# Performance work log

Hardware: AMD Instinct MI355X
Metric: run time of the kernel (lower is better)

Reference implementation:

```python
import jax, jax.numpy as jnp
import numpy as np

N = 100000   # nodes
E = 500000   # edges
D = 128      # h_dim
R = 230      # relation types ('num_edges' in __init__)
B = 64       # num_bases
SI = D // B  # submat_in = 2
SO = D // B  # submat_out = 2
L = 2        # n_hidden_layers
RRELU_SLOPE = (1.0 / 8.0 + 1.0 / 3.0) / 2.0  # F.rrelu eval-mode negative slope


def setup_inputs() -> dict:
    key = jax.random.key(0)
    ks = jax.random.split(key, 9)
    ent_embeds = jax.random.normal(ks[0], (N, D), jnp.float32)
    rel_embeds = jax.random.normal(ks[1], (R, D), jnp.float32)
    # xavier_normal-ish scale for per-relation basis weights and self-loop weights
    weight = jax.random.normal(ks[2], (L, R, B * SI * SO), jnp.float32) * 0.1
    loop_weight = jax.random.normal(ks[3], (L, D, D), jnp.float32) * (2.0 / np.sqrt(2 * D))
    norm = jax.random.uniform(ks[4], (N, 1), jnp.float32)
    node_id = jax.random.randint(ks[5], (N,), 0, N)
    edge_type = jax.random.randint(ks[6], (E,), 0, R)
    src = jax.random.randint(ks[7], (E,), 0, N)
    dst = jax.random.randint(ks[8], (E,), 0, N)
    return dict(ent_embeds=ent_embeds, rel_embeds=rel_embeds, weight=weight,
                loop_weight=loop_weight, norm=norm, node_id=node_id,
                edge_type=edge_type, src=src, dst=dst)


def reference(ent_embeds, rel_embeds, weight, loop_weight, norm,
              node_id, edge_type, src, dst):
    # Aggregator.forward: h = ent_embeds[g.ndata['id']]
    h = ent_embeds[node_id]  # [N, D]
    # (rel_embeds are gathered into g.edata['h'] but unused by RGCNLayer)
    for l in range(L):
        # msg_func: per-edge basis-block weight gather + block-diag bmm
        w = weight[l][edge_type].reshape(E, B, SI, SO)   # [E, B, 2, 2]
        node = h[src].reshape(E, B, SI)                  # [E, B, 2]
        msg = jnp.einsum('ebi,ebio->ebo', node, w).reshape(E, D)
        # update_all scatter-sum + apply_func norm multiply
        agg = jax.ops.segment_sum(msg, dst, num_segments=N) * norm
        # self-loop message (dropout=0)
        agg = agg + h @ loop_weight[l]
        # F.rrelu in eval mode: leaky with slope (lower+upper)/2
        h = jnp.where(agg >= 0, agg, agg * RRELU_SLOPE)
    return h
```

## Files before the change

kernel.cpp:

```cpp
#include <hip/hip_runtime.h>
#include <hip/hip_bf16.h>

#define NN 100000
#define NE 500000
#define DD 128
#define RR 230
#define SLOPE 0.2291666666666666667f

typedef __attribute__((ext_vector_type(8))) short short8;
typedef __attribute__((ext_vector_type(4))) float f32x4;

__device__ __forceinline__ short f2bf(float f) {
    unsigned u = __float_as_uint(f);
    u += 0x7fffu + ((u >> 16) & 1u);
    return (short)(u >> 16);
}
__device__ __forceinline__ unsigned pkbf(float lo, float hi) {
    return (unsigned)(unsigned short)f2bf(lo) | ((unsigned)(unsigned short)f2bf(hi) << 16);
}

#if defined(__has_builtin)
#if __has_builtin(__builtin_amdgcn_fdot2_f32_bf16)
#define HAS_DOT2 1
#endif
#endif
__device__ __forceinline__ void dot2acc(float& acc, unsigned x, unsigned w) {
#ifdef HAS_DOT2
    typedef __attribute__((ext_vector_type(2))) __bf16 bf16x2;
    acc = __builtin_amdgcn_fdot2_f32_bf16(__builtin_bit_cast(bf16x2, x),
                                          __builtin_bit_cast(bf16x2, w), acc, false);
#else
    acc = fmaf(__uint_as_float(x << 16),        __uint_as_float(w << 16),
          fmaf(__uint_as_float(x & 0xFFFF0000u), __uint_as_float(w & 0xFFFF0000u), acc));
#endif
}

__global__ __launch_bounds__(256) void hprep_k(const float* __restrict__ ent,
                                               const int* __restrict__ nid,
                                               unsigned short* __restrict__ hb) {
    int gid = blockIdx.x * 256 + threadIdx.x;
    if (gid >= (NN + 1) * 16) return;
    int n = gid >> 4;
    int u = gid & 15;
    short8 v = {0, 0, 0, 0, 0, 0, 0, 0};
    if (n < NN) {
        const float* srcp = ent + (size_t)nid[n] * DD + u * 8;
        float4 f0 = *(const float4*)srcp;
        float4 f1 = *(const float4*)(srcp + 4);
        v[0] = f2bf(f0.x); v[1] = f2bf(f0.y); v[2] = f2bf(f0.z); v[3] = f2bf(f0.w);
        v[4] = f2bf(f1.x); v[5] = f2bf(f1.y); v[6] = f2bf(f1.z); v[7] = f2bf(f1.w);
    }
    *(short8*)(hb + (size_t)n * DD + u * 8) = v;
}

__global__ __launch_bounds__(256) void hist_k(const int* __restrict__ dst,
                                              int* __restrict__ cnt) {
    int e = blockIdx.x * 256 + threadIdx.x;
    if (e >= NE) return;
    atomicAdd(&cnt[dst[e]], 1);
}

__global__ __launch_bounds__(256) void scan1_k(const int* __restrict__ cnt,
                                               int* __restrict__ off,
                                               int* __restrict__ bsum) {
    __shared__ int sh[256];
    int i = blockIdx.x * 256 + threadIdx.x;
    int v = (i < NN) ? cnt[i] : 0;
    sh[threadIdx.x] = v;
    __syncthreads();
    for (int d = 1; d < 256; d <<= 1) {
        int t = (threadIdx.x >= d) ? sh[threadIdx.x - d] : 0;
        __syncthreads();
        sh[threadIdx.x] += t;
        __syncthreads();
    }
    if (i < NN) off[i] = sh[threadIdx.x] - v;
    if (threadIdx.x == 255) bsum[blockIdx.x] = sh[255];
}

__global__ __launch_bounds__(512) void scan2_k(int* __restrict__ bsum, int nb) {
    __shared__ int sh[512];
    int v = (threadIdx.x < nb) ? bsum[threadIdx.x] : 0;
    sh[threadIdx.x] = v;
    __syncthreads();
    for (int d = 1; d < 512; d <<= 1) {
        int t = (threadIdx.x >= d) ? sh[threadIdx.x - d] : 0;
        __syncthreads();
        sh[threadIdx.x] += t;
        __syncthreads();
    }
    if (threadIdx.x < nb) bsum[threadIdx.x] = sh[threadIdx.x] - v;
}

__global__ __launch_bounds__(256) void scan3_k(int* __restrict__ off,
                                               const int* __restrict__ bsum,
                                               int* __restrict__ cursor) {
    int i = blockIdx.x * 256 + threadIdx.x;
    if (i < NN) {
        int o = off[i] + bsum[blockIdx.x];
        off[i] = o;
        cursor[i] = o;
    }
    if (i == 0) off[NN] = NE;
}

__global__ __launch_bounds__(256) void scat_k(const int* __restrict__ src,
                                              const int* __restrict__ et,
                                              const int* __restrict__ dst,
                                              int* __restrict__ cursor,
                                              int* __restrict__ epack) {
    int e = blockIdx.x * 256 + threadIdx.x;
    if (e >= NE) return;
    int pos = atomicAdd(&cursor[dst[e]], 1);
    epack[pos] = (src[e] << 8) | et[e];
}

__global__ __launch_bounds__(256) void wbprep_k(const float* __restrict__ weight,
                                                unsigned* __restrict__ wb) {
    int gid = blockIdx.x * 256 + threadIdx.x;
    if (gid >= 2 * RR * 32) return;
    int lt = gid >> 5;
    int hl = gid & 31;
    const float* wsrc = weight + (size_t)lt * 256 + hl * 8;
    float4 f0 = *(const float4*)wsrc;
    float4 f1 = *(const float4*)(wsrc + 4);
    uint4 v;
    v.x = pkbf(f0.x, f0.z);
    v.y = pkbf(f0.y, f0.w);
    v.z = pkbf(f1.x, f1.z);
    v.w = pkbf(f1.y, f1.w);
    *(uint4*)(wb + (size_t)lt * 128 + hl * 4) = v;
}

__global__ __launch_bounds__(256) void wprep_k(const float* __restrict__ lw,
                                               short* __restrict__ wt) {
    int gid = blockIdx.x * 256 + threadIdx.x;
    if (gid >= 2 * DD * 16) return;
    int l   = gid >> 11;
    int rem = gid & 2047;
    int c   = rem >> 4;
    int u   = rem & 15;
    const float* wsrc = lw + l * DD * DD + c;
    short8 v;
    #pragma unroll
    for (int j = 0; j < 8; ++j) v[j] = f2bf(wsrc[(u * 8 + j) * DD]);
    *(short8*)(wt + (size_t)l * DD * DD + c * DD + ((u ^ (c & 7)) << 3)) = v;
}

#define ZP (NN << 8)
__global__ __launch_bounds__(256) void agg_k(const unsigned short* __restrict__ hb,
                                             const int* __restrict__ off,
                                             const int* __restrict__ epack,
                                             const unsigned* __restrict__ wb,
                                             const float* __restrict__ norm,
                                             unsigned short* __restrict__ aggb) {
    int n    = (blockIdx.x * 256 + threadIdx.x) >> 6;
    int lane = threadIdx.x & 63;
    int hl   = lane & 31;
    int h2   = lane >> 5;
    if (n >= NN) return;
    int e0 = off[n];
    int m  = off[n + 1] - e0;
    float a0 = 0.f, a1 = 0.f, a2 = 0.f, a3 = 0.f;
    const char* hbb = (const char*)hb;
    const char* wbb = (const char*)wb;
    const int hoff = hl * 8;
    const int woff = hl * 16;

    for (int base = 0; base < m; base += 64) {
        int cnt = m - base;
        if (cnt > 64) cnt = 64;
        int pv = epack[e0 + base + ((lane < cnt) ? lane : 0)];

        for (int j = 0; j < cnt; j += 8) {
            int i0 = j + h2, i1 = j + 2 + h2, i2 = j + 4 + h2, i3 = j + 6 + h2;
            int p0 = (i0 < cnt) ? __shfl(pv, i0) : ZP;
            int p1 = (i1 < cnt) ? __shfl(pv, i1) : ZP;
            int p2 = (i2 < cnt) ? __shfl(pv, i2) : ZP;
            int p3 = (i3 < cnt) ? __shfl(pv, i3) : ZP;
            uint2 x0 = *(const uint2*)(hbb + (p0 & 0xFFFFFF00u) + hoff);
            uint2 x1 = *(const uint2*)(hbb + (p1 & 0xFFFFFF00u) + hoff);
            uint2 x2 = *(const uint2*)(hbb + (p2 & 0xFFFFFF00u) + hoff);
            uint2 x3 = *(const uint2*)(hbb + (p3 & 0xFFFFFF00u) + hoff);
            uint4 w0 = *(const uint4*)(wbb + ((p0 & 255) << 9) + woff);
            uint4 w1 = *(const uint4*)(wbb + ((p1 & 255) << 9) + woff);
            uint4 w2 = *(const uint4*)(wbb + ((p2 & 255) << 9) + woff);
            uint4 w3 = *(const uint4*)(wbb + ((p3 & 255) << 9) + woff);
            dot2acc(a0, x0.x, w0.x); dot2acc(a1, x0.x, w0.y);
            dot2acc(a2, x0.y, w0.z); dot2acc(a3, x0.y, w0.w);
            dot2acc(a0, x1.x, w1.x); dot2acc(a1, x1.x, w1.y);
            dot2acc(a2, x1.y, w1.z); dot2acc(a3, x1.y, w1.w);
            dot2acc(a0, x2.x, w2.x); dot2acc(a1, x2.x, w2.y);
            dot2acc(a2, x2.y, w2.z); dot2acc(a3, x2.y, w2.w);
            dot2acc(a0, x3.x, w3.x); dot2acc(a1, x3.x, w3.y);
            dot2acc(a2, x3.y, w3.z); dot2acc(a3, x3.y, w3.w);
        }
    }
    a0 += __shfl_xor(a0, 32);
    a1 += __shfl_xor(a1, 32);
    a2 += __shfl_xor(a2, 32);
    a3 += __shfl_xor(a3, 32);
    if (h2 == 0) {
        float nv = norm[n];
        uint2 pk;
        pk.x = pkbf(a0 * nv, a1 * nv);
        pk.y = pkbf(a2 * nv, a3 * nv);
        *(uint2*)(aggb + (size_t)n * DD + hl * 4) = pk;
    }
}

template<int WRITE_BF16>
__global__ __launch_bounds__(256, 2) void apply_k(const unsigned short* __restrict__ aggb,
                                                  const unsigned short* __restrict__ hb,
                                                  const short* __restrict__ Wt,
                                                  float* __restrict__ outf,
                                                  unsigned short* __restrict__ outb) {
    __shared__ short Ash[DD * DD];
    __shared__ short Wsh[DD * DD];

    const int tid = threadIdx.x;
    const long n0 = (long)blockIdx.x * 128;

    {
        const float4* wsrc = (const float4*)Wt;
        float4*       wdst = (float4*)Wsh;
        #pragma unroll
        for (int i = 0; i < 8; ++i) wdst[tid + i * 256] = wsrc[tid + i * 256];
    }
    {
        const int r  = tid >> 1;
        const int hf = tid & 1;
        long srow = n0 + r;
        if (srow >= NN) srow = NN - 1;
        const unsigned short* hrow = hb + (size_t)srow * DD + hf * 64;
        short* arow = Ash + r * DD;
        #pragma unroll
        for (int uu = 0; uu < 8; ++uu) {
            int u = hf * 8 + uu;
            short8 v = *(const short8*)(hrow + uu * 8);
            *(short8*)(arow + ((u ^ (r & 7)) << 3)) = v;
        }
    }
    __syncthreads();

    const int wv  = tid >> 6;
    const int wm  = wv >> 1;
    const int wn  = wv & 1;
    const int l16 = tid & 15;
    const int q   = (tid & 63) >> 4;

    f32x4 acc[4][4];
    #pragma unroll
    for (int mt = 0; mt < 4; ++mt)
        #pragma unroll
        for (int nt = 0; nt < 4; ++nt) acc[mt][nt] = (f32x4){0.f, 0.f, 0.f, 0.f};

    union Frag { uint2 u2[2]; short8 s8; };

    #pragma unroll
    for (int ks = 0; ks < 4; ++ks) {
        const int ua   = ks * 4 + (q >> 1);
        const int off8 = 4 * (q & 1);
        short8 af[4], bf[4];
        #pragma unroll
        for (int mt = 0; mt < 4; ++mt) {
            int r = wm * 64 + mt * 16 + l16;
            const short* base = Ash + r * DD;
            Frag fr;
            fr.u2[0] = *(const uint2*)(base + ((ua       ^ (r & 7)) << 3) + off8);
            fr.u2[1] = *(const uint2*)(base + (((ua + 2) ^ (r & 7)) << 3) + off8);
            af[mt] = fr.s8;
        }
        #pragma unroll
        for (int nt = 0; nt < 4; ++nt) {
            int c = wn * 64 + nt * 16 + l16;
            const short* base = Wsh + c * DD;
            Frag fr;
            fr.u2[0] = *(const uint2*)(base + ((ua       ^ (c & 7)) << 3) + off8);
            fr.u2[1] = *(const uint2*)(base + (((ua + 2) ^ (c & 7)) << 3) + off8);
            bf[nt] = fr.s8;
        }
        #pragma unroll
        for (int mt = 0; mt < 4; ++mt)
            #pragma unroll
            for (int nt = 0; nt < 4; ++nt)
                acc[mt][nt] = __builtin_amdgcn_mfma_f32_16x16x32_bf16(
                                  af[mt], bf[nt], acc[mt][nt], 0, 0, 0);
    }

    #pragma unroll
    for (int mt = 0; mt < 4; ++mt) {
        #pragma unroll
        for (int i = 0; i < 4; ++i) {
            long nrow = n0 + wm * 64 + mt * 16 + 4 * q + i;
            if (nrow < NN) {
                #pragma unroll
                for (int nt = 0; nt < 4; ++nt) {
                    int c = wn * 64 + nt * 16 + l16;
                    float g = __uint_as_float((unsigned)aggb[nrow * DD + c] << 16);
                    float v = g + acc[mt][nt][i];
                    v = (v >= 0.f) ? v : v * SLOPE;
                    if (WRITE_BF16) outb[nrow * DD + c] = (unsigned short)f2bf(v);
                    else            outf[nrow * DD + c] = v;
                }
            }
        }
    }
}

extern "C" void kernel_launch(void* const* d_in, const int* in_sizes, int n_in,
                              void* d_out, int out_size, void* d_ws, size_t ws_size,
                              hipStream_t stream) {
    const float* ent_embeds  = (const float*)d_in[0];
    const float* weight      = (const float*)d_in[2];
    const float* loop_weight = (const float*)d_in[3];
    const float* norm        = (const float*)d_in[4];
    const int*   node_id     = (const int*)d_in[5];
    const int*   edge_type   = (const int*)d_in[6];
    const int*   src         = (const int*)d_in[7];
    const int*   dst         = (const int*)d_in[8];
    float*       out         = (float*)d_out;

    unsigned short* aggb = (unsigned short*)d_ws;
    unsigned short* hb   = aggb + (size_t)NN * DD;
    int*   cnt    = (int*)(hb + (size_t)(NN + 1) * DD);
    int*   off    = cnt + NN;
    int*   cursor = off + NN + 1;
    int*   bsum   = cursor + NN;
    int*   epack  = bsum + 512;
    short* wt     = (short*)(epack + NE);
    unsigned* wb  = (unsigned*)(wt + 2 * DD * DD);

    const int NB_E = (NE + 255) / 256;
    const int NB_N = (NN + 255) / 256;

    hipMemsetAsync(cnt, 0, (size_t)NN * sizeof(int), stream);
    wprep_k <<<16, 256, 0, stream>>>(loop_weight, wt);
    wbprep_k<<<(2 * RR * 32 + 255) / 256, 256, 0, stream>>>(weight, wb);
    hprep_k <<<((NN + 1) * 16 + 255) / 256, 256, 0, stream>>>(ent_embeds, node_id, hb);
    hist_k  <<<NB_E, 256, 0, stream>>>(dst, cnt);
    scan1_k <<<NB_N, 256, 0, stream>>>(cnt, off, bsum);
    scan2_k <<<1,    512, 0, stream>>>(bsum, NB_N);
    scan3_k <<<NB_N, 256, 0, stream>>>(off, bsum, cursor);
    scat_k  <<<NB_E, 256, 0, stream>>>(src, edge_type, dst, cursor, epack);

    const int AGG_BLOCKS = (NN * 64) / 256;
    const int APL_BLOCKS = (NN + 127) / 128;

    agg_k     <<<AGG_BLOCKS, 256, 0, stream>>>(hb, off, epack, wb, norm, aggb);
    apply_k<1><<<APL_BLOCKS, 256, 0, stream>>>(aggb, hb, wt, nullptr, hb);

    agg_k     <<<AGG_BLOCKS, 256, 0, stream>>>(hb, off, epack, wb + (size_t)RR * 128,
                                               norm, aggb);
    apply_k<0><<<APL_BLOCKS, 256, 0, stream>>>(aggb, hb, wt + (size_t)DD * DD, out, nullptr);
}
```

Before: 212.5 us.

## Merge prep kernels, fuse scan stages, pad CSR segments to multiples of eight

Four preprocessing kernels (loop-weight transpose, basis-weight pack, h gather/convert, degree histogram) are merged into one launch that also fills a padded edge buffer with a zero-row sentinel. The scan now rounds each node's degree up to a multiple of eight, and the second and third scan stages are folded into one kernel where each block reduces the preceding block sums itself. The aggregation loop drops its per-64 chunking and bounds checks, loading eight packed edges per step and relying on the sentinel padding. The aim is fewer launches and a simpler inner loop, at the cost of a larger edge buffer, an extra fill pass and wasted work on padded slots.

```diff
diff --git a/kernel.cpp b/kernel.cpp
--- a/kernel.cpp
+++ b/kernel.cpp
@@ -6,6 +6,9 @@
 #define DD 128
 #define RR 230
 #define SLOPE 0.2291666666666666667f
+
+#define EPMAX (NE + 7 * NN)
+#define ZP (NN << 8)
 
 typedef __attribute__((ext_vector_type(8))) short short8;
 typedef __attribute__((ext_vector_type(4))) float f32x4;
@@ -35,29 +38,73 @@
 #endif
 }
 
-__global__ __launch_bounds__(256) void hprep_k(const float* __restrict__ ent,
-                                               const int* __restrict__ nid,
-                                               unsigned short* __restrict__ hb) {
-    int gid = blockIdx.x * 256 + threadIdx.x;
-    if (gid >= (NN + 1) * 16) return;
-    int n = gid >> 4;
-    int u = gid & 15;
-    short8 v = {0, 0, 0, 0, 0, 0, 0, 0};
-    if (n < NN) {
-        const float* srcp = ent + (size_t)nid[n] * DD + u * 8;
-        float4 f0 = *(const float4*)srcp;
-        float4 f1 = *(const float4*)(srcp + 4);
-        v[0] = f2bf(f0.x); v[1] = f2bf(f0.y); v[2] = f2bf(f0.z); v[3] = f2bf(f0.w);
-        v[4] = f2bf(f1.x); v[5] = f2bf(f1.y); v[6] = f2bf(f1.z); v[7] = f2bf(f1.w);
-    }
-    *(short8*)(hb + (size_t)n * DD + u * 8) = v;
-}
-
-__global__ __launch_bounds__(256) void hist_k(const int* __restrict__ dst,
-                                              int* __restrict__ cnt) {
-    int e = blockIdx.x * 256 + threadIdx.x;
-    if (e >= NE) return;
-    atomicAdd(&cnt[dst[e]], 1);
+#define P1_WT_E   16
+#define P1_WB_E   74
+#define P1_FL_E   (74 + (EPMAX / 4 + 255) / 256)
+#define P1_HB_E   (P1_FL_E + ((NN + 1) * 16 + 255) / 256)
+#define P1_TOT    (P1_HB_E + (NE + 255) / 256)
+
+__global__ __launch_bounds__(256) void p1_k(const float* __restrict__ lw,
+                                            const float* __restrict__ weight,
+                                            const float* __restrict__ ent,
+                                            const int* __restrict__ nid,
+                                            const int* __restrict__ dst,
+                                            short* __restrict__ wt,
+                                            unsigned* __restrict__ wb,
+                                            unsigned short* __restrict__ hb,
+                                            int* __restrict__ epack,
+                                            int* __restrict__ cnt) {
+    int bid = blockIdx.x;
+    if (bid < P1_WT_E) {
+        int gid = bid * 256 + threadIdx.x;
+        if (gid >= 2 * DD * 16) return;
+        int l   = gid >> 11;
+        int rem = gid & 2047;
+        int c   = rem >> 4;
+        int u   = rem & 15;
+        const float* wsrc = lw + l * DD * DD + c;
+        short8 v;
+        #pragma unroll
+        for (int j = 0; j < 8; ++j) v[j] = f2bf(wsrc[(u * 8 + j) * DD]);
+        *(short8*)(wt + (size_t)l * DD * DD + c * DD + ((u ^ (c & 7)) << 3)) = v;
+    } else if (bid < P1_WB_E) {
+        int gid = (bid - P1_WT_E) * 256 + threadIdx.x;
+        if (gid >= 2 * RR * 32) return;
+        int lt = gid >> 5;
+        int hl = gid & 31;
+        const float* wsrc = weight + (size_t)lt * 256 + hl * 8;
+        float4 f0 = *(const float4*)wsrc;
+        float4 f1 = *(const float4*)(wsrc + 4);
+        uint4 v;
+        v.x = pkbf(f0.x, f0.z);
+        v.y = pkbf(f0.y, f0.w);
+        v.z = pkbf(f1.x, f1.z);
+        v.w = pkbf(f1.y, f1.w);
+        *(uint4*)(wb + (size_t)lt * 128 + hl * 4) = v;
+    } else if (bid < P1_FL_E) {
+        int idx = (bid - P1_WB_E) * 256 + threadIdx.x;
+        if (idx * 4 >= EPMAX) return;
+        int4 z = make_int4(ZP, ZP, ZP, ZP);
+        *(int4*)(epack + idx * 4) = z;
+    } else if (bid < P1_HB_E) {
+        int gid = (bid - P1_FL_E) * 256 + threadIdx.x;
+        if (gid >= (NN + 1) * 16) return;
+        int n = gid >> 4;
+        int u = gid & 15;
+        short8 v = {0, 0, 0, 0, 0, 0, 0, 0};
+        if (n < NN) {
+            const float* srcp = ent + (size_t)nid[n] * DD + u * 8;
+            float4 f0 = *(const float4*)srcp;
+            float4 f1 = *(const float4*)(srcp + 4);
+            v[0] = f2bf(f0.x); v[1] = f2bf(f0.y); v[2] = f2bf(f0.z); v[3] = f2bf(f0.w);
+            v[4] = f2bf(f1.x); v[5] = f2bf(f1.y); v[6] = f2bf(f1.z); v[7] = f2bf(f1.w);
+        }
+        *(short8*)(hb + (size_t)n * DD + u * 8) = v;
+    } else {
+        int e = (bid - P1_HB_E) * 256 + threadIdx.x;
+        if (e >= NE) return;
+        atomicAdd(&cnt[dst[e]], 1);
+    }
 }
 
 __global__ __launch_bounds__(256) void scan1_k(const int* __restrict__ cnt,
@@ -65,7 +112,7 @@
                                                int* __restrict__ bsum) {
     __shared__ int sh[256];
     int i = blockIdx.x * 256 + threadIdx.x;
-    int v = (i < NN) ? cnt[i] : 0;
+    int v = (i < NN) ? ((cnt[i] + 7) & ~7) : 0;
     sh[threadIdx.x] = v;
     __syncthreads();
     for (int d = 1; d < 256; d <<= 1) {
@@ -78,30 +125,31 @@
     if (threadIdx.x == 255) bsum[blockIdx.x] = sh[255];
 }
 
-__global__ __launch_bounds__(512) void scan2_k(int* __restrict__ bsum, int nb) {
-    __shared__ int sh[512];
-    int v = (threadIdx.x < nb) ? bsum[threadIdx.x] : 0;
-    sh[threadIdx.x] = v;
+__global__ __launch_bounds__(256) void scan23_k(int* __restrict__ off,
+                                                const int* __restrict__ bsum,
+                                                int* __restrict__ cursor,
+                                                int nb) {
+    __shared__ int sh[256];
+    const int bid = blockIdx.x;
+    const int tid = threadIdx.x;
+    int s = 0;
+    if (tid < bid) s = bsum[tid];
+    if (tid + 256 < bid) s += bsum[tid + 256];
+    sh[tid] = s;
     __syncthreads();
-    for (int d = 1; d < 512; d <<= 1) {
-        int t = (threadIdx.x >= d) ? sh[threadIdx.x - d] : 0;
+    #pragma unroll
+    for (int d = 128; d > 0; d >>= 1) {
+        if (tid < d) sh[tid] += sh[tid + d];
         __syncthreads();
-        sh[threadIdx.x] += t;
-        __syncthreads();
-    }
-    if (threadIdx.x < nb) bsum[threadIdx.x] = sh[threadIdx.x] - v;
-}
-
-__global__ __launch_bounds__(256) void scan3_k(int* __restrict__ off,
-                                               const int* __restrict__ bsum,
-                                               int* __restrict__ cursor) {
-    int i = blockIdx.x * 256 + threadIdx.x;
+    }
+    const int S = sh[0];
+    int i = bid * 256 + tid;
     if (i < NN) {
-        int o = off[i] + bsum[blockIdx.x];
+        int o = off[i] + S;
         off[i] = o;
         cursor[i] = o;
     }
-    if (i == 0) off[NN] = NE;
+    if (bid == nb - 1 && tid == 0) off[NN] = S + bsum[bid];
 }
 
 __global__ __launch_bounds__(256) void scat_k(const int* __restrict__ src,
@@ -115,39 +163,6 @@
     epack[pos] = (src[e] << 8) | et[e];
 }
 
-__global__ __launch_bounds__(256) void wbprep_k(const float* __restrict__ weight,
-                                                unsigned* __restrict__ wb) {
-    int gid = blockIdx.x * 256 + threadIdx.x;
-    if (gid >= 2 * RR * 32) return;
-    int lt = gid >> 5;
-    int hl = gid & 31;
-    const float* wsrc = weight + (size_t)lt * 256 + hl * 8;
-    float4 f0 = *(const float4*)wsrc;
-    float4 f1 = *(const float4*)(wsrc + 4);
-    uint4 v;
-    v.x = pkbf(f0.x, f0.z);
-    v.y = pkbf(f0.y, f0.w);
-    v.z = pkbf(f1.x, f1.z);
-    v.w = pkbf(f1.y, f1.w);
-    *(uint4*)(wb + (size_t)lt * 128 + hl * 4) = v;
-}
-
-__global__ __launch_bounds__(256) void wprep_k(const float* __restrict__ lw,
-                                               short* __restrict__ wt) {
-    int gid = blockIdx.x * 256 + threadIdx.x;
-    if (gid >= 2 * DD * 16) return;
-    int l   = gid >> 11;
-    int rem = gid & 2047;
-    int c   = rem >> 4;
-    int u   = rem & 15;
-    const float* wsrc = lw + l * DD * DD + c;
-    short8 v;
-    #pragma unroll
-    for (int j = 0; j < 8; ++j) v[j] = f2bf(wsrc[(u * 8 + j) * DD]);
-    *(short8*)(wt + (size_t)l * DD * DD + c * DD + ((u ^ (c & 7)) << 3)) = v;
-}
-
-#define ZP (NN << 8)
 __global__ __launch_bounds__(256) void agg_k(const unsigned short* __restrict__ hb,
                                              const int* __restrict__ off,
                                              const int* __restrict__ epack,
@@ -161,47 +176,39 @@
     if (n >= NN) return;
     int e0 = off[n];
     int m  = off[n + 1] - e0;
+    float nv = norm[n];
     float a0 = 0.f, a1 = 0.f, a2 = 0.f, a3 = 0.f;
-    const char* hbb = (const char*)hb;
-    const char* wbb = (const char*)wb;
-    const int hoff = hl * 8;
-    const int woff = hl * 16;
-
-    for (int base = 0; base < m; base += 64) {
-        int cnt = m - base;
-        if (cnt > 64) cnt = 64;
-        int pv = epack[e0 + base + ((lane < cnt) ? lane : 0)];
-
-        for (int j = 0; j < cnt; j += 8) {
-            int i0 = j + h2, i1 = j + 2 + h2, i2 = j + 4 + h2, i3 = j + 6 + h2;
-            int p0 = (i0 < cnt) ? __shfl(pv, i0) : ZP;
-            int p1 = (i1 < cnt) ? __shfl(pv, i1) : ZP;
-            int p2 = (i2 < cnt) ? __shfl(pv, i2) : ZP;
-            int p3 = (i3 < cnt) ? __shfl(pv, i3) : ZP;
-            uint2 x0 = *(const uint2*)(hbb + (p0 & 0xFFFFFF00u) + hoff);
-            uint2 x1 = *(const uint2*)(hbb + (p1 & 0xFFFFFF00u) + hoff);
-            uint2 x2 = *(const uint2*)(hbb + (p2 & 0xFFFFFF00u) + hoff);
-            uint2 x3 = *(const uint2*)(hbb + (p3 & 0xFFFFFF00u) + hoff);
-            uint4 w0 = *(const uint4*)(wbb + ((p0 & 255) << 9) + woff);
-            uint4 w1 = *(const uint4*)(wbb + ((p1 & 255) << 9) + woff);
-            uint4 w2 = *(const uint4*)(wbb + ((p2 & 255) << 9) + woff);
-            uint4 w3 = *(const uint4*)(wbb + ((p3 & 255) << 9) + woff);
-            dot2acc(a0, x0.x, w0.x); dot2acc(a1, x0.x, w0.y);
-            dot2acc(a2, x0.y, w0.z); dot2acc(a3, x0.y, w0.w);
-            dot2acc(a0, x1.x, w1.x); dot2acc(a1, x1.x, w1.y);
-            dot2acc(a2, x1.y, w1.z); dot2acc(a3, x1.y, w1.w);
-            dot2acc(a0, x2.x, w2.x); dot2acc(a1, x2.x, w2.y);
-            dot2acc(a2, x2.y, w2.z); dot2acc(a3, x2.y, w2.w);
-            dot2acc(a0, x3.x, w3.x); dot2acc(a1, x3.x, w3.y);
-            dot2acc(a2, x3.y, w3.z); dot2acc(a3, x3.y, w3.w);
-        }
+    const char* hbb = (const char*)hb + hl * 8;
+    const char* wbb = (const char*)wb + hl * 16;
+
+    for (int j = 0; j < m; j += 8) {
+        int pv = epack[e0 + j + (lane & 7)];
+        int p0 = __shfl(pv, h2);
+        int p1 = __shfl(pv, 2 + h2);
+        int p2 = __shfl(pv, 4 + h2);
+        int p3 = __shfl(pv, 6 + h2);
+        uint2 x0 = *(const uint2*)(hbb + (p0 & 0xFFFFFF00u));
+        uint2 x1 = *(const uint2*)(hbb + (p1 & 0xFFFFFF00u));
+        uint2 x2 = *(const uint2*)(hbb + (p2 & 0xFFFFFF00u));
+        uint2 x3 = *(const uint2*)(hbb + (p3 & 0xFFFFFF00u));
+        uint4 w0 = *(const uint4*)(wbb + ((p0 & 255) << 9));
+        uint4 w1 = *(const uint4*)(wbb + ((p1 & 255) << 9));
+        uint4 w2 = *(const uint4*)(wbb + ((p2 & 255) << 9));
+        uint4 w3 = *(const uint4*)(wbb + ((p3 & 255) << 9));
+        dot2acc(a0, x0.x, w0.x); dot2acc(a1, x0.x, w0.y);
+        dot2acc(a2, x0.y, w0.z); dot2acc(a3, x0.y, w0.w);
+        dot2acc(a0, x1.x, w1.x); dot2acc(a1, x1.x, w1.y);
+        dot2acc(a2, x1.y, w1.z); dot2acc(a3, x1.y, w1.w);
+        dot2acc(a0, x2.x, w2.x); dot2acc(a1, x2.x, w2.y);
+        dot2acc(a2, x2.y, w2.z); dot2acc(a3, x2.y, w2.w);
+        dot2acc(a0, x3.x, w3.x); dot2acc(a1, x3.x, w3.y);
+        dot2acc(a2, x3.y, w3.z); dot2acc(a3, x3.y, w3.w);
     }
     a0 += __shfl_xor(a0, 32);
     a1 += __shfl_xor(a1, 32);
     a2 += __shfl_xor(a2, 32);
     a3 += __shfl_xor(a3, 32);
     if (h2 == 0) {
-        float nv = norm[n];
         uint2 pk;
         pk.x = pkbf(a0 * nv, a1 * nv);
         pk.y = pkbf(a2 * nv, a3 * nv);
@@ -326,22 +333,19 @@
     int*   cnt    = (int*)(hb + (size_t)(NN + 1) * DD);
     int*   off    = cnt + NN;
     int*   cursor = off + NN + 1;
-    int*   bsum   = cursor + NN;
-    int*   epack  = bsum + 512;
-    short* wt     = (short*)(epack + NE);
+    int*   epack  = cursor + NN;
+    int*   bsum   = epack + EPMAX;
+    short* wt     = (short*)(bsum + 512);
     unsigned* wb  = (unsigned*)(wt + 2 * DD * DD);
 
     const int NB_E = (NE + 255) / 256;
     const int NB_N = (NN + 255) / 256;
 
     hipMemsetAsync(cnt, 0, (size_t)NN * sizeof(int), stream);
-    wprep_k <<<16, 256, 0, stream>>>(loop_weight, wt);
-    wbprep_k<<<(2 * RR * 32 + 255) / 256, 256, 0, stream>>>(weight, wb);
-    hprep_k <<<((NN + 1) * 16 + 255) / 256, 256, 0, stream>>>(ent_embeds, node_id, hb);
-    hist_k  <<<NB_E, 256, 0, stream>>>(dst, cnt);
+    p1_k    <<<P1_TOT, 256, 0, stream>>>(loop_weight, weight, ent_embeds, node_id, dst,
+                                         wt, wb, hb, epack, cnt);
     scan1_k <<<NB_N, 256, 0, stream>>>(cnt, off, bsum);
-    scan2_k <<<1,    512, 0, stream>>>(bsum, NB_N);
-    scan3_k <<<NB_N, 256, 0, stream>>>(off, bsum, cursor);
+    scan23_k<<<NB_N, 256, 0, stream>>>(off, bsum, cursor, NB_N);
     scat_k  <<<NB_E, 256, 0, stream>>>(src, edge_type, dst, cursor, epack);
 
     const int AGG_BLOCKS = (NN * 64) / 256;
```

Measured after the change: 198.8 us. -6.4%, faster.
